# Optimization experiments

Measured on AMD Instinct MI355X. Metric: run time of the kernel, lower is better.

## Reference

```python
import jax, jax.numpy as jnp
import numpy as np

NEG_SLOPE = 0.2   # PyG GATConv leaky_relu slope
BN_EPS = 1e-5
N_NODES, N_EDGES = 50000, 800000
HEADS, CH, EDGE_DIM, K = 4, 64, 3, 4


def _bn(x):
    # BatchNorm1d in training mode, gamma=1, beta=0 (init defaults)
    mu = x.mean(axis=0)
    var = x.var(axis=0)
    return (x - mu) / jnp.sqrt(var + BN_EPS)


def _gat(x, src, dst, ea, W, a_src, a_dst, We, a_edge, bias, heads, out_ch):
    """PyG-style GATConv with edge features, add_self_loops=True (fill_value='mean')."""
    N = x.shape[0]
    E = src.shape[0]
    # self-loop edge_attr = scatter-mean of edge_attr by dst
    deg = jax.ops.segment_sum(jnp.ones((E,), x.dtype), dst, num_segments=N)
    ea_loop = jax.ops.segment_sum(ea, dst, num_segments=N) / jnp.maximum(deg, 1.0)[:, None]
    loop = jnp.arange(N)
    src2 = jnp.concatenate([src, loop])
    dst2 = jnp.concatenate([dst, loop])
    ea2 = jnp.concatenate([ea, ea_loop], axis=0)          # (E+N, edge_dim)
    h = (x @ W).reshape(N, heads, out_ch)                  # (N,H,C)
    a_s = (h * a_src).sum(-1)                              # (N,H)
    a_d = (h * a_dst).sum(-1)                              # (N,H)
    eh = (ea2 @ We).reshape(-1, heads, out_ch)             # (E+N,H,C)
    a_e = (eh * a_edge).sum(-1)                            # (E+N,H)
    logit = jax.nn.leaky_relu(a_s[src2] + a_d[dst2] + a_e, NEG_SLOPE)
    m = jax.lax.stop_gradient(jax.ops.segment_max(logit, dst2, num_segments=N))
    ex = jnp.exp(logit - m[dst2])
    den = jax.ops.segment_sum(ex, dst2, num_segments=N)
    alpha = ex / (den[dst2] + 1e-16)                       # segment softmax over dst
    out = jax.ops.segment_sum(alpha[:, :, None] * h[src2], dst2, num_segments=N)
    return out.reshape(N, heads * out_ch) + bias


def setup_inputs() -> dict:
    key = jax.random.key(0)
    ks = jax.random.split(key, 24)
    N, E, H, C, ED = N_NODES, N_EDGES, HEADS, CH, EDGE_DIM

    def g(k, shape, s=0.05):
        return jax.random.normal(k, shape, jnp.float32) * s

    return {
        "x": jax.random.normal(ks[0], (N, 2), jnp.float32),
        "edge_index": jax.random.randint(ks[1], (2, E), 0, N),
        "edge_attr": jax.random.normal(ks[2], (E, ED), jnp.float32),
        "Wp": g(ks[3], (2, C)), "bp": jnp.zeros((C,), jnp.float32),
        "W1": g(ks[4], (C, H * C)), "as1": g(ks[5], (H, C)), "ad1": g(ks[6], (H, C)),
        "We1": g(ks[7], (ED, H * C)), "ae1": g(ks[8], (H, C)), "b1": jnp.zeros((H * C,), jnp.float32),
        "W2": g(ks[9], (H * C, H * C)), "as2": g(ks[10], (H, C)), "ad2": g(ks[11], (H, C)),
        "We2": g(ks[12], (ED, H * C)), "ae2": g(ks[13], (H, C)), "b2": jnp.zeros((H * C,), jnp.float32),
        "W3": g(ks[14], (H * C, C)), "as3": g(ks[15], (1, C)), "ad3": g(ks[16], (1, C)),
        "We3": g(ks[17], (ED, C)), "ae3": g(ks[18], (1, C)), "b3": jnp.zeros((C,), jnp.float32),
        "Wc": g(ks[19], (C, K)), "bc": jnp.zeros((K,), jnp.float32),
    }


def reference(x, edge_index, edge_attr, Wp, bp,
              W1, as1, ad1, We1, ae1, b1,
              W2, as2, ad2, We2, ae2, b2,
              W3, as3, ad3, We3, ae3, b3,
              Wc, bc):
    src, dst = edge_index[0], edge_index[1]
    h = jax.nn.elu(_bn(x @ Wp + bp))
    h = jax.nn.elu(_bn(_gat(h, src, dst, edge_attr, W1, as1, ad1, We1, ae1, b1, HEADS, CH)))
    h = jax.nn.elu(_bn(_gat(h, src, dst, edge_attr, W2, as2, ad2, We2, ae2, b2, HEADS, CH)))
    h = jax.nn.elu(_gat(h, src, dst, edge_attr, W3, as3, ad3, We3, ae3, b3, 1, CH))
    logits = h @ Wc + bc
    return jax.nn.softmax(logits / 1.0, axis=-1)  # temperature = 1.0
```

## Files before the change

kernel.cpp:

```cpp
#include <hip/hip_runtime.h>
#include <hip/hip_fp16.h>
#include <math.h>

#define NN 50000
#define NE 800000
#define NEG 0.2f
#define EPS_BN 1e-5f
#define NROW 8192
#define NB_SC ((NN + 255) / 256)

typedef _Float16 f16x8 __attribute__((ext_vector_type(8)));
typedef float f32x4 __attribute__((ext_vector_type(4)));

struct __align__(16) Edge { int s; float e0, e1, e2; };

__device__ __forceinline__ float lrelu(float x){ return x > 0.f ? x : NEG * x; }
__device__ __forceinline__ float elu(float x){ return x > 0.f ? x : expm1f(x); }

__global__ __launch_bounds__(256) void k_deg(const int* __restrict__ dst, int* __restrict__ deg){
  int e = blockIdx.x * 256 + threadIdx.x;
  if (e >= NE) return;
  atomicAdd(&deg[dst[e]], 1);
}

__global__ __launch_bounds__(256) void k_scan1(const int* __restrict__ deg, int* __restrict__ bsum){
  __shared__ int sd[4];
  int t = threadIdx.x;
  int i = blockIdx.x * 256 + t;
  int v = (i < NN) ? deg[i] : 0;
  int s = v;
#pragma unroll
  for (int off = 32; off; off >>= 1) s += __shfl_down(s, off, 64);
  if ((t & 63) == 0) sd[t >> 6] = s;
  __syncthreads();
  if (t == 0) bsum[blockIdx.x] = sd[0] + sd[1] + sd[2] + sd[3];
}

__global__ __launch_bounds__(256) void k_scan2(int* __restrict__ bsum, int* __restrict__ rowptr){
  __shared__ int sm[256];
  int t = threadIdx.x;
  int v = (t < NB_SC) ? bsum[t] : 0;
  sm[t] = v;
  __syncthreads();
  for (int off = 1; off < 256; off <<= 1){
    int p = (t >= off) ? sm[t - off] : 0;
    __syncthreads();
    sm[t] += p;
    __syncthreads();
  }
  if (t < NB_SC) bsum[t] = sm[t] - v;
  if (t == 0) rowptr[NN] = NE;
}

__global__ __launch_bounds__(256) void k_scan3(const int* __restrict__ deg, const int* __restrict__ bsum,
                                               int* __restrict__ rowptr){
  __shared__ int sm[256];
  int t = threadIdx.x;
  int i = blockIdx.x * 256 + t;
  int v = (i < NN) ? deg[i] : 0;
  sm[t] = v;
  __syncthreads();
  for (int off = 1; off < 256; off <<= 1){
    int p = (t >= off) ? sm[t - off] : 0;
    __syncthreads();
    sm[t] += p;
    __syncthreads();
  }
  if (i < NN) rowptr[i] = bsum[blockIdx.x] + sm[t] - v;
}

__global__ __launch_bounds__(256) void k_fill(const int* __restrict__ src, const int* __restrict__ dst,
                                              const float* __restrict__ ea, const int* __restrict__ rowptr,
                                              int* __restrict__ cnt, Edge* __restrict__ edges){
  int e = blockIdx.x * 256 + threadIdx.x;
  if (e >= NE) return;
  int d = dst[e];
  int pos = rowptr[d] + atomicAdd(&cnt[d], 1);
  Edge ed;
  ed.s = src[e];
  ed.e0 = ea[e*3+0]; ed.e1 = ea[e*3+1]; ed.e2 = ea[e*3+2];
  edges[pos] = ed;
}

__global__ __launch_bounds__(256) void k_easum(const int* __restrict__ rowptr, const Edge* __restrict__ edges,
                                               float* __restrict__ easum){
  int n = blockIdx.x * 4 + (threadIdx.x >> 6);
  int c = threadIdx.x & 63;
  if (n >= NN) return;
  int start = rowptr[n], end = rowptr[n + 1];
  float s0 = 0.f, s1 = 0.f, s2 = 0.f;
  for (int p = start + c; p < end; p += 64){
    Edge e = edges[p];
    s0 += e.e0; s1 += e.e1; s2 += e.e2;
  }
#pragma unroll
  for (int off = 32; off; off >>= 1){
    s0 += __shfl_down(s0, off, 64);
    s1 += __shfl_down(s1, off, 64);
    s2 += __shfl_down(s2, off, 64);
  }
  if (c == 0){ easum[n*3+0] = s0; easum[n*3+1] = s1; easum[n*3+2] = s2; }
}

__global__ __launch_bounds__(256) void k_proj(const float* __restrict__ x, const float* __restrict__ Wp,
                                              const float* __restrict__ bp, float* __restrict__ h0){
  int i = blockIdx.x * 256 + threadIdx.x;
  if (i >= NN * 64) return;
  int n = i >> 6, c = i & 63;
  h0[i] = fmaf(x[n*2+0], Wp[c], fmaf(x[n*2+1], Wp[64+c], bp[c]));
}

template<int F>
__global__ void k_bn_stats(const float* __restrict__ x, float* __restrict__ ps, float* __restrict__ pq){
  int t = threadIdx.x;
  float s = 0.f, s2 = 0.f;
  for (int n = blockIdx.x; n < NN; n += 512){
    float v = x[(long)n * F + t];
    s += v; s2 += v * v;
  }
  ps[blockIdx.x * F + t] = s;
  pq[blockIdx.x * F + t] = s2;
}

template<int F>
__global__ void k_bn_fin(const float* __restrict__ ps, const float* __restrict__ pq,
                         float* __restrict__ mu, float* __restrict__ rs){
  int t = threadIdx.x;
  float s = 0.f, s2 = 0.f;
  for (int b = 0; b < 512; b++){ s += ps[b * F + t]; s2 += pq[b * F + t]; }
  float m = s * (1.f / NN);
  float var = s2 * (1.f / NN) - m * m;
  mu[t] = m;
  rs[t] = rsqrtf(var + EPS_BN);
}

__global__ __launch_bounds__(256) void k_wt(const float* __restrict__ W, __half* __restrict__ Wt,
                                            int K, int J){
  int t = blockIdx.x * 256 + threadIdx.x;
  if (t >= K * J) return;
  int k = t / J, j = t % J;
  Wt[(long)j * K + k] = __float2half(W[t]);
}

template<int H>
__global__ void k_edge_g(const float* __restrict__ We, const float* __restrict__ ae, float* __restrict__ g){
  int t = threadIdx.x;
  int h = t >> 6, c = t & 63;
  float a = ae[t];
  for (int d = 0; d < 3; d++){
    float p = We[d * (H*64) + t] * a;
    for (int off = 32; off; off >>= 1) p += __shfl_down(p, off, 64);
    if (c == 0) g[d * H + h] = p;
  }
  (void)h;
}

template<int K, int J>
__global__ __launch_bounds__(256) void k_gemm_mfma(const float* __restrict__ A, const __half* __restrict__ Wt,
                                                   const float* __restrict__ mu, const float* __restrict__ rs,
                                                   const float* __restrict__ asrc, const float* __restrict__ adst,
                                                   __half* __restrict__ C, float* __restrict__ aS,
                                                   float* __restrict__ aD){
  constexpr int NS = J / 16;
  constexpr int KT = K / 32;
  constexpr int HH = J / 64;
  __shared__ __half Bs[J][40];
  int t = threadIdx.x;
  int w = t >> 6;
  int l = t & 63;
  int row0 = blockIdx.x * 64;
  int lr = l & 15;
  int lg = l >> 4;

  f32x4 acc[NS];
#pragma unroll
  for (int s = 0; s < NS; s++) acc[s] = (f32x4){0.f, 0.f, 0.f, 0.f};

  int arow = row0 + w * 16 + lr;
  bool aval = arow < NN;
  const float* Arow = A + (long)arow * K;

  auto loadA = [&](int kt) -> f16x8 {
    f16x8 r;
#pragma unroll
    for (int k = 0; k < 8; k++) r[k] = (_Float16)0.f;
    if (aval){
      int k0 = kt * 32 + lg * 8;
      float4 q0 = *(const float4*)&Arow[k0];
      float4 q1 = *(const float4*)&Arow[k0 + 4];
      float4 m0 = *(const float4*)&mu[k0];
      float4 m1 = *(const float4*)&mu[k0 + 4];
      float4 r0 = *(const float4*)&rs[k0];
      float4 r1 = *(const float4*)&rs[k0 + 4];
      r[0] = (_Float16)elu((q0.x - m0.x) * r0.x);
      r[1] = (_Float16)elu((q0.y - m0.y) * r0.y);
      r[2] = (_Float16)elu((q0.z - m0.z) * r0.z);
      r[3] = (_Float16)elu((q0.w - m0.w) * r0.w);
      r[4] = (_Float16)elu((q1.x - m1.x) * r1.x);
      r[5] = (_Float16)elu((q1.y - m1.y) * r1.y);
      r[6] = (_Float16)elu((q1.z - m1.z) * r1.z);
      r[7] = (_Float16)elu((q1.w - m1.w) * r1.w);
    }
    return r;
  };

  f16x8 af_cur = loadA(0);

  for (int kt = 0; kt < KT; kt++){
    int kk = kt * 32;
#pragma unroll
    for (int i = 0; i < J / 64; i++){
      int ch = t + 256 * i;
      int c = ch >> 2, q = ch & 3;
      *(uint4*)&Bs[c][q * 8] = *(const uint4*)(Wt + (long)c * K + kk + q * 8);
    }
    __syncthreads();
    f16x8 af_nxt;
#pragma unroll
    for (int k = 0; k < 8; k++) af_nxt[k] = (_Float16)0.f;
    if (kt + 1 < KT) af_nxt = loadA(kt + 1);
#pragma unroll
    for (int s = 0; s < NS; s++){
      f16x8 bf = *(const f16x8*)&Bs[s * 16 + lr][lg * 8];
      acc[s] = __builtin_amdgcn_mfma_f32_16x16x32_f16(af_cur, bf, acc[s], 0, 0, 0);
    }
    __syncthreads();
    af_cur = af_nxt;
  }

  int orow = row0 + w * 16 + lg * 4;
  float sA[HH][4], dA[HH][4];
#pragma unroll
  for (int hd = 0; hd < HH; hd++)
#pragma unroll
    for (int i = 0; i < 4; i++){ sA[hd][i] = 0.f; dA[hd][i] = 0.f; }

#pragma unroll
  for (int s = 0; s < NS; s++){
    int cidx = s * 16 + lr;
    int hd = s >> 2;
    float a1 = asrc[cidx], a2 = adst[cidx];
#pragma unroll
    for (int i = 0; i < 4; i++){
      float v = acc[s][i];
      sA[hd][i] = fmaf(v, a1, sA[hd][i]);
      dA[hd][i] = fmaf(v, a2, dA[hd][i]);
      int r = orow + i;
      if (r < NN) C[(long)r * J + cidx] = __float2half(v);
    }
  }
#pragma unroll
  for (int off = 1; off <= 8; off <<= 1){
#pragma unroll
    for (int hd = 0; hd < HH; hd++)
#pragma unroll
      for (int i = 0; i < 4; i++){
        sA[hd][i] += __shfl_xor(sA[hd][i], off, 64);
        dA[hd][i] += __shfl_xor(dA[hd][i], off, 64);
      }
  }
  if (lr == 0){
#pragma unroll
    for (int i = 0; i < 4; i++){
      int r = orow + i;
      if (r < NN){
#pragma unroll
        for (int hd = 0; hd < HH; hd++){
          aS[r * HH + hd] = sA[hd][i];
          aD[r * HH + hd] = dA[hd][i];
        }
      }
    }
  }
}

__global__ __launch_bounds__(256) void k_gatn(const int* __restrict__ rowptr, const Edge* __restrict__ edges,
                                              const int* __restrict__ deg, const float* __restrict__ easum,
                                              const float* __restrict__ aS, const float* __restrict__ aD,
                                              const float* __restrict__ g4, const __half* __restrict__ hh,
                                              const float* __restrict__ bias, float* __restrict__ out){
  const int W = 256;
  int wid = threadIdx.x >> 6;
  int lane = threadIdx.x & 63;
  int row = blockIdx.x * 4 + wid;
  int e4 = lane >> 2, hl = lane & 3;
  int es = lane >> 5, ch8 = lane & 31;
  int c = ch8 * 8;
  int h2 = ch8 >> 3;
  float g0 = g4[0*4+hl], g1 = g4[1*4+hl], g2 = g4[2*4+hl];
  float4 bb0 = *(const float4*)&bias[c];
  float4 bb1 = *(const float4*)&bias[c+4];

  for (int n = row; n < NN; n += NROW){
    int start = rowptr[n], end = rowptr[n+1];
    float adn = aD[n*4+hl];
    float dg = (float)deg[n];
    float inv = 1.f / fmaxf(dg, 1.f);
    float ll = aS[n*4+hl] + adn + g0*(easum[n*3+0]*inv) + g1*(easum[n*3+1]*inv) + g2*(easum[n*3+2]*inv);
    ll = lrelu(ll);
    float evl = __expf(ll);
    float evl2 = __shfl(evl, h2, 64);
    f16x8 sv = *(const f16x8*)(hh + (long)n * W + c);
    float acc[8];
#pragma unroll
    for (int k = 0; k < 8; k++) acc[k] = (es == 0) ? evl2 * (float)sv[k] : 0.f;
    float denp = (lane < 4) ? evl : 0.f;

    for (int b0 = start; b0 < end; b0 += 16){
      int len = end - b0; if (len > 16) len = 16;
      float ev = 0.f; unsigned pk = 0;
      if (e4 < len){
        Edge e = edges[b0 + e4];
        float l = lrelu(aS[e.s*4+hl] + adn + g0*e.e0 + g1*e.e1 + g2*e.e2);
        ev = __expf(l);
        pk = ((unsigned)e.s << 16) | (unsigned)__half_as_ushort(__float2half(ev));
      }
      denp += ev;
      int iters = (len + 1) >> 1;
      for (int i = 0; i < iters; i++){
        int j = i * 2 + es;
        bool valid = j < len;
        int jj = valid ? j : 0;
        unsigned pj = __shfl((int)pk, jj * 4 + h2, 64);
        float aj = valid ? __half2float(__ushort_as_half((unsigned short)(pj & 0xffffu))) : 0.f;
        int sj = (int)(pj >> 16);
        f16x8 v = *(const f16x8*)(hh + (long)sj * W + c);
#pragma unroll
        for (int k = 0; k < 8; k++) acc[k] = fmaf(aj, (float)v[k], acc[k]);
      }
    }
#pragma unroll
    for (int off = 4; off <= 32; off <<= 1) denp += __shfl_xor(denp, off, 64);
    float den2 = __shfl(denp, h2, 64);
#pragma unroll
    for (int k = 0; k < 8; k++) acc[k] += __shfl_xor(acc[k], 32, 64);
    if (es == 0){
      float invd = 1.f / (den2 + 1e-16f);
      float o[8];
      o[0] = fmaf(acc[0], invd, bb0.x); o[1] = fmaf(acc[1], invd, bb0.y);
      o[2] = fmaf(acc[2], invd, bb0.z); o[3] = fmaf(acc[3], invd, bb0.w);
      o[4] = fmaf(acc[4], invd, bb1.x); o[5] = fmaf(acc[5], invd, bb1.y);
      o[6] = fmaf(acc[6], invd, bb1.z); o[7] = fmaf(acc[7], invd, bb1.w);
      *(float4*)&out[(long)n * W + c]     = make_float4(o[0], o[1], o[2], o[3]);
      *(float4*)&out[(long)n * W + c + 4] = make_float4(o[4], o[5], o[6], o[7]);
    }
  }
}

template<int H, bool ELU>
__global__ __launch_bounds__(256) void k_gatw(const int* __restrict__ rowptr, const Edge* __restrict__ edges,
                                              const int* __restrict__ deg, const float* __restrict__ easum,
                                              const float* __restrict__ aS, const float* __restrict__ aD,
                                              const float* __restrict__ g, const __half* __restrict__ hh,
                                              const float* __restrict__ bias, float* __restrict__ out){
  constexpr int W = H * 64;
  int wid = threadIdx.x >> 6;
  int lane = threadIdx.x & 63;
  int n = blockIdx.x * 4 + wid;
  int h = 0;
  if (n >= NN) return;
  int start = rowptr[n], end = rowptr[n + 1];
  float g0 = g[0*H+h], g1 = g[1*H+h], g2 = g[2*H+h];
  float adn = aD[n*H+h];
  int ch8 = lane >> 3;
  int es = lane & 7;

  float dg = (float)deg[n];
  float inv = 1.f / fmaxf(dg, 1.f);
  float ll = aS[n*H+h] + adn + g0*(easum[n*3+0]*inv) + g1*(easum[n*3+1]*inv) + g2*(easum[n*3+2]*inv);
  ll = lrelu(ll);
  float evl = __expf(ll);
  f16x8 sv = *(const f16x8*)(hh + (long)n * W + h * 64 + ch8 * 8);
  float acc[8];
#pragma unroll
  for (int k = 0; k < 8; k++) acc[k] = (es == 0) ? evl * (float)sv[k] : 0.f;
  float denp = (lane == 0) ? evl : 0.f;

  for (int base0 = start; base0 < end; base0 += 64){
    int len = end - base0; if (len > 64) len = 64;
    float ev = 0.f;
    unsigned pk = 0;
    if (lane < len){
      Edge e = edges[base0 + lane];
      float l = lrelu(aS[e.s*H+h] + adn + g0*e.e0 + g1*e.e1 + g2*e.e2);
      ev = __expf(l);
      pk = ((unsigned)e.s << 16) | (unsigned)__half_as_ushort(__float2half(ev));
    }
    denp += ev;
    for (int j = es; j < len; j += 8){
      unsigned pj = __shfl((int)pk, j, 64);
      float aj = __half2float(__ushort_as_half((unsigned short)(pj & 0xffffu)));
      int sj = (int)(pj >> 16);
      f16x8 v = *(const f16x8*)(hh + (long)sj * W + h * 64 + ch8 * 8);
#pragma unroll
      for (int k = 0; k < 8; k++) acc[k] = fmaf(aj, (float)v[k], acc[k]);
    }
  }

#pragma unroll
  for (int off = 32; off; off >>= 1) denp += __shfl_xor(denp, off, 64);
#pragma unroll
  for (int k = 0; k < 8; k++){
    acc[k] += __shfl_xor(acc[k], 1, 64);
    acc[k] += __shfl_xor(acc[k], 2, 64);
    acc[k] += __shfl_xor(acc[k], 4, 64);
  }
  if (es == 0){
    float invden = 1.f / (denp + 1e-16f);
    int cb = h * 64 + ch8 * 8;
    float4 b0 = *(const float4*)&bias[cb];
    float4 b1 = *(const float4*)&bias[cb + 4];
    float bb[8] = {b0.x, b0.y, b0.z, b0.w, b1.x, b1.y, b1.z, b1.w};
#pragma unroll
    for (int k = 0; k < 8; k++){
      acc[k] = acc[k] * invden + bb[k];
      if (ELU) acc[k] = acc[k] > 0.f ? acc[k] : expm1f(acc[k]);
    }
    float4 o0 = make_float4(acc[0], acc[1], acc[2], acc[3]);
    float4 o1 = make_float4(acc[4], acc[5], acc[6], acc[7]);
    *(float4*)&out[(long)n * W + cb] = o0;
    *(float4*)&out[(long)n * W + cb + 4] = o1;
  }
}

__global__ __launch_bounds__(64) void k_final(const float* __restrict__ h3, const float* __restrict__ Wc,
                                              const float* __restrict__ bc, float* __restrict__ out){
  int n = blockIdx.x;
  int c = threadIdx.x;
  float v = h3[(long)n * 64 + c];
  float r0 = v * Wc[c*4+0], r1 = v * Wc[c*4+1], r2 = v * Wc[c*4+2], r3 = v * Wc[c*4+3];
  for (int off = 32; off; off >>= 1){
    r0 += __shfl_down(r0, off, 64);
    r1 += __shfl_down(r1, off, 64);
    r2 += __shfl_down(r2, off, 64);
    r3 += __shfl_down(r3, off, 64);
  }
  if (c == 0){
    r0 += bc[0]; r1 += bc[1]; r2 += bc[2]; r3 += bc[3];
    float mm = fmaxf(fmaxf(r0, r1), fmaxf(r2, r3));
    float e0 = __expf(r0 - mm), e1 = __expf(r1 - mm), e2 = __expf(r2 - mm), e3 = __expf(r3 - mm);
    float is = 1.f / (e0 + e1 + e2 + e3);
    out[n*4+0] = e0 * is; out[n*4+1] = e1 * is; out[n*4+2] = e2 * is; out[n*4+3] = e3 * is;
  }
}

extern "C" void kernel_launch(void* const* d_in, const int* in_sizes, int n_in,
                              void* d_out, int out_size, void* d_ws, size_t ws_size,
                              hipStream_t stream){
  const float* x   = (const float*)d_in[0];
  const int*   ei  = (const int*)d_in[1];
  const float* ea  = (const float*)d_in[2];
  const float* Wp  = (const float*)d_in[3];
  const float* bp  = (const float*)d_in[4];
  const float* W1  = (const float*)d_in[5];
  const float* as1 = (const float*)d_in[6];
  const float* ad1 = (const float*)d_in[7];
  const float* We1 = (const float*)d_in[8];
  const float* ae1 = (const float*)d_in[9];
  const float* b1  = (const float*)d_in[10];
  const float* W2  = (const float*)d_in[11];
  const float* as2 = (const float*)d_in[12];
  const float* ad2 = (const float*)d_in[13];
  const float* We2 = (const float*)d_in[14];
  const float* ae2 = (const float*)d_in[15];
  const float* b2  = (const float*)d_in[16];
  const float* W3  = (const float*)d_in[17];
  const float* as3 = (const float*)d_in[18];
  const float* ad3 = (const float*)d_in[19];
  const float* We3 = (const float*)d_in[20];
  const float* ae3 = (const float*)d_in[21];
  const float* b3  = (const float*)d_in[22];
  const float* Wc  = (const float*)d_in[23];
  const float* bc  = (const float*)d_in[24];
  const int* srcI = ei;
  const int* dstI = ei + NE;

  char* base = (char*)d_ws;
  size_t off = 0;
  auto alloc = [&](size_t bytes) -> void* {
    void* p = base + off;
    off += (bytes + 255) & ~(size_t)255;
    return p;
  };
  float*  bufA  = (float*)alloc((size_t)NN * 256 * 4);
  __half* hB    = (__half*)alloc((size_t)NN * 256 * 2);
  __half* Wt1   = (__half*)alloc((size_t)64 * 256 * 2);
  __half* Wt2   = (__half*)alloc((size_t)256 * 256 * 2);
  __half* Wt3   = (__half*)alloc((size_t)256 * 64 * 2);
  int*   deg   = (int*)  alloc((size_t)NN * 4);
  int*   cnt   = (int*)  alloc((size_t)NN * 4);
  int*   rowptr= (int*)  alloc((size_t)(NN + 1) * 4);
  int*   bsum  = (int*)  alloc((size_t)NB_SC * 4);
  Edge*  edges = (Edge*) alloc((size_t)NE * sizeof(Edge));
  float* easum = (float*)alloc((size_t)NN * 3 * 4);
  float* aS    = (float*)alloc((size_t)NN * 4 * 4);
  float* aD    = (float*)alloc((size_t)NN * 4 * 4);
  float* g     = (float*)alloc(256);
  float* pbs   = (float*)alloc((size_t)512 * 256 * 4);
  float* pbq   = (float*)alloc((size_t)512 * 256 * 4);
  float* bmu   = (float*)alloc(256 * 4);
  float* brs   = (float*)alloc(256 * 4);
  (void)ws_size; (void)in_sizes; (void)n_in; (void)out_size;

  hipMemsetAsync(deg, 0, (size_t)NN * 4, stream);
  hipMemsetAsync(cnt, 0, (size_t)NN * 4, stream);
  k_deg<<<(NE + 255) / 256, 256, 0, stream>>>(dstI, deg);
  k_scan1<<<NB_SC, 256, 0, stream>>>(deg, bsum);
  k_scan2<<<1, 256, 0, stream>>>(bsum, rowptr);
  k_scan3<<<NB_SC, 256, 0, stream>>>(deg, bsum, rowptr);
  k_fill<<<(NE + 255) / 256, 256, 0, stream>>>(srcI, dstI, ea, rowptr, cnt, edges);
  k_easum<<<(NN + 3) / 4, 256, 0, stream>>>(rowptr, edges, easum);
  k_wt<<<(64 * 256 + 255) / 256, 256, 0, stream>>>(W1, Wt1, 64, 256);
  k_wt<<<(256 * 256 + 255) / 256, 256, 0, stream>>>(W2, Wt2, 256, 256);
  k_wt<<<(256 * 64 + 255) / 256, 256, 0, stream>>>(W3, Wt3, 256, 64);

  k_proj<<<(NN * 64 + 255) / 256, 256, 0, stream>>>(x, Wp, bp, bufA);
  k_bn_stats<64><<<512, 64, 0, stream>>>(bufA, pbs, pbq);
  k_bn_fin<64><<<1, 64, 0, stream>>>(pbs, pbq, bmu, brs);

  k_edge_g<4><<<1, 256, 0, stream>>>(We1, ae1, g);
  k_gemm_mfma<64, 256><<<(NN + 63) / 64, 256, 0, stream>>>(bufA, Wt1, bmu, brs, as1, ad1, hB, aS, aD);
  k_gatn<<<NROW / 4, 256, 0, stream>>>(rowptr, edges, deg, easum, aS, aD, g, hB, b1, bufA);
  k_bn_stats<256><<<512, 256, 0, stream>>>(bufA, pbs, pbq);
  k_bn_fin<256><<<1, 256, 0, stream>>>(pbs, pbq, bmu, brs);

  k_edge_g<4><<<1, 256, 0, stream>>>(We2, ae2, g);
  k_gemm_mfma<256, 256><<<(NN + 63) / 64, 256, 0, stream>>>(bufA, Wt2, bmu, brs, as2, ad2, hB, aS, aD);
  k_gatn<<<NROW / 4, 256, 0, stream>>>(rowptr, edges, deg, easum, aS, aD, g, hB, b2, bufA);
  k_bn_stats<256><<<512, 256, 0, stream>>>(bufA, pbs, pbq);
  k_bn_fin<256><<<1, 256, 0, stream>>>(pbs, pbq, bmu, brs);

  k_edge_g<1><<<1, 64, 0, stream>>>(We3, ae3, g);
  k_gemm_mfma<256, 64><<<(NN + 63) / 64, 256, 0, stream>>>(bufA, Wt3, bmu, brs, as3, ad3, hB, aS, aD);
  k_gatw<1, true><<<(NN + 3) / 4, 256, 0, stream>>>(rowptr, edges, deg, easum, aS, aD, g, hB, b3, bufA);

  k_final<<<NN, 64, 0, stream>>>(bufA, Wc, bc, (float*)d_out);
}
```

Baseline: 550.3 us.

## Fuse BatchNorm statistics into GAT aggregation kernel and merge weight transposes

Each GAT aggregation kernel now accumulates per-channel sum and sum-of-squares of its outputs, reduces them across the block's waves in shared memory, and writes per-block partials. A new parallel finalize kernel (one block per channel) reduces those partials into mean and rsqrt variance. This removes the separate BN-stats pass that re-read the 50000x256 fp32 output after each of the first two GAT layers. The three weight-transpose launches are also merged into one. The cost is extra registers in the GAT kernel and a larger partial buffer to reduce.

After: 500.3 us. -9.1%, faster.

```diff
diff --git a/kernel.cpp b/kernel.cpp
--- a/kernel.cpp
+++ b/kernel.cpp
@@ -7,6 +7,7 @@
 #define NEG 0.2f
 #define EPS_BN 1e-5f
 #define NROW 8192
+#define NGB  (NROW / 4)
 #define NB_SC ((NN + 255) / 256)
 
 typedef _Float16 f16x8 __attribute__((ext_vector_type(8)));
@@ -134,12 +135,43 @@
   rs[t] = rsqrtf(var + EPS_BN);
 }
 
-__global__ __launch_bounds__(256) void k_wt(const float* __restrict__ W, __half* __restrict__ Wt,
-                                            int K, int J){
+__global__ __launch_bounds__(256) void k_bn_fin2048(const float* __restrict__ pbs, const float* __restrict__ pbq,
+                                                    float* __restrict__ mu, float* __restrict__ rs){
+  __shared__ float sd[2][4];
+  int c = blockIdx.x;
+  int t = threadIdx.x;
+  float s = 0.f, q = 0.f;
+  for (int i = t; i < NGB; i += 256){ s += pbs[c * NGB + i]; q += pbq[c * NGB + i]; }
+#pragma unroll
+  for (int off = 32; off; off >>= 1){ s += __shfl_down(s, off, 64); q += __shfl_down(q, off, 64); }
+  if ((t & 63) == 0){ sd[0][t >> 6] = s; sd[1][t >> 6] = q; }
+  __syncthreads();
+  if (t == 0){
+    s = sd[0][0] + sd[0][1] + sd[0][2] + sd[0][3];
+    q = sd[1][0] + sd[1][1] + sd[1][2] + sd[1][3];
+    float m = s * (1.f / NN);
+    float var = q * (1.f / NN) - m * m;
+    mu[c] = m;
+    rs[c] = rsqrtf(var + EPS_BN);
+  }
+}
+
+__global__ __launch_bounds__(256) void k_wt3(const float* __restrict__ W1, const float* __restrict__ W2,
+                                             const float* __restrict__ W3, __half* __restrict__ Wt1,
+                                             __half* __restrict__ Wt2, __half* __restrict__ Wt3){
   int t = blockIdx.x * 256 + threadIdx.x;
-  if (t >= K * J) return;
-  int k = t / J, j = t % J;
-  Wt[(long)j * K + k] = __float2half(W[t]);
+  if (t < 64 * 256){
+    int k = t / 256, j = t % 256;
+    Wt1[(long)j * 64 + k] = __float2half(W1[t]);
+  }
+  if (t < 256 * 256){
+    int k = t / 256, j = t % 256;
+    Wt2[(long)j * 256 + k] = __float2half(W2[t]);
+  }
+  if (t < 256 * 64){
+    int k = t / 64, j = t % 64;
+    Wt3[(long)j * 256 + k] = __float2half(W3[t]);
+  }
 }
 
 template<int H>
@@ -274,11 +306,13 @@
   }
 }
 
+template<bool STATS>
 __global__ __launch_bounds__(256) void k_gatn(const int* __restrict__ rowptr, const Edge* __restrict__ edges,
                                               const int* __restrict__ deg, const float* __restrict__ easum,
                                               const float* __restrict__ aS, const float* __restrict__ aD,
                                               const float* __restrict__ g4, const __half* __restrict__ hh,
-                                              const float* __restrict__ bias, float* __restrict__ out){
+                                              const float* __restrict__ bias, float* __restrict__ out,
+                                              float* __restrict__ pbs, float* __restrict__ pbq){
   const int W = 256;
   int wid = threadIdx.x >> 6;
   int lane = threadIdx.x & 63;
@@ -290,6 +324,11 @@
   float g0 = g4[0*4+hl], g1 = g4[1*4+hl], g2 = g4[2*4+hl];
   float4 bb0 = *(const float4*)&bias[c];
   float4 bb1 = *(const float4*)&bias[c+4];
+  float sum8[8], sq8[8];
+  if (STATS){
+#pragma unroll
+    for (int k = 0; k < 8; k++){ sum8[k] = 0.f; sq8[k] = 0.f; }
+  }
 
   for (int n = row; n < NN; n += NROW){
     int start = rowptr[n], end = rowptr[n+1];
@@ -341,9 +380,28 @@
       o[2] = fmaf(acc[2], invd, bb0.z); o[3] = fmaf(acc[3], invd, bb0.w);
       o[4] = fmaf(acc[4], invd, bb1.x); o[5] = fmaf(acc[5], invd, bb1.y);
       o[6] = fmaf(acc[6], invd, bb1.z); o[7] = fmaf(acc[7], invd, bb1.w);
+      if (STATS){
+#pragma unroll
+        for (int k = 0; k < 8; k++){ sum8[k] += o[k]; sq8[k] += o[k]*o[k]; }
+      }
       *(float4*)&out[(long)n * W + c]     = make_float4(o[0], o[1], o[2], o[3]);
       *(float4*)&out[(long)n * W + c + 4] = make_float4(o[4], o[5], o[6], o[7]);
     }
+  }
+
+  if (STATS){
+    __shared__ float ls[4][256];
+    __shared__ float lq[4][256];
+    if (es == 0){
+#pragma unroll
+      for (int k = 0; k < 8; k++){ ls[wid][c + k] = sum8[k]; lq[wid][c + k] = sq8[k]; }
+    }
+    __syncthreads();
+    int ch = threadIdx.x;
+    float s = ls[0][ch] + ls[1][ch] + ls[2][ch] + ls[3][ch];
+    float q = lq[0][ch] + lq[1][ch] + lq[2][ch] + lq[3][ch];
+    pbs[ch * NGB + blockIdx.x] = s;
+    pbq[ch * NGB + blockIdx.x] = q;
   }
 }
 
@@ -496,8 +554,8 @@
   float* aS    = (float*)alloc((size_t)NN * 4 * 4);
   float* aD    = (float*)alloc((size_t)NN * 4 * 4);
   float* g     = (float*)alloc(256);
-  float* pbs   = (float*)alloc((size_t)512 * 256 * 4);
-  float* pbq   = (float*)alloc((size_t)512 * 256 * 4);
+  float* pbs   = (float*)alloc((size_t)256 * NGB * 4);
+  float* pbq   = (float*)alloc((size_t)256 * NGB * 4);
   float* bmu   = (float*)alloc(256 * 4);
   float* brs   = (float*)alloc(256 * 4);
   (void)ws_size; (void)in_sizes; (void)n_in; (void)out_size;
@@ -510,9 +568,7 @@
   k_scan3<<<NB_SC, 256, 0, stream>>>(deg, bsum, rowptr);
   k_fill<<<(NE + 255) / 256, 256, 0, stream>>>(srcI, dstI, ea, rowptr, cnt, edges);
   k_easum<<<(NN + 3) / 4, 256, 0, stream>>>(rowptr, edges, easum);
-  k_wt<<<(64 * 256 + 255) / 256, 256, 0, stream>>>(W1, Wt1, 64, 256);
-  k_wt<<<(256 * 256 + 255) / 256, 256, 0, stream>>>(W2, Wt2, 256, 256);
-  k_wt<<<(256 * 64 + 255) / 256, 256, 0, stream>>>(W3, Wt3, 256, 64);
+  k_wt3<<<(256 * 256 + 255) / 256, 256, 0, stream>>>(W1, W2, W3, Wt1, Wt2, Wt3);
 
   k_proj<<<(NN * 64 + 255) / 256, 256, 0, stream>>>(x, Wp, bp, bufA);
   k_bn_stats<64><<<512, 64, 0, stream>>>(bufA, pbs, pbq);
@@ -520,15 +576,13 @@
 
   k_edge_g<4><<<1, 256, 0, stream>>>(We1, ae1, g);
   k_gemm_mfma<64, 256><<<(NN + 63) / 64, 256, 0, stream>>>(bufA, Wt1, bmu, brs, as1, ad1, hB, aS, aD);
-  k_gatn<<<NROW / 4, 256, 0, stream>>>(rowptr, edges, deg, easum, aS, aD, g, hB, b1, bufA);
-  k_bn_stats<256><<<512, 256, 0, stream>>>(bufA, pbs, pbq);
-  k_bn_fin<256><<<1, 256, 0, stream>>>(pbs, pbq, bmu, brs);
+  k_gatn<true><<<NGB, 256, 0, stream>>>(rowptr, edges, deg, easum, aS, aD, g, hB, b1, bufA, pbs, pbq);
+  k_bn_fin2048<<<256, 256, 0, stream>>>(pbs, pbq, bmu, brs);
 
   k_edge_g<4><<<1, 256, 0, stream>>>(We2, ae2, g);
   k_gemm_mfma<256, 256><<<(NN + 63) / 64, 256, 0, stream>>>(bufA, Wt2, bmu, brs, as2, ad2, hB, aS, aD);
-  k_gatn<<<NROW / 4, 256, 0, stream>>>(rowptr, edges, deg, easum, aS, aD, g, hB, b2, bufA);
-  k_bn_stats<256><<<512, 256, 0, stream>>>(bufA, pbs, pbq);
-  k_bn_fin<256><<<1, 256, 0, stream>>>(pbs, pbq, bmu, brs);
+  k_gatn<true><<<NGB, 256, 0, stream>>>(rowptr, edges, deg, easum, aS, aD, g, hB, b2, bufA, pbs, pbq);
+  k_bn_fin2048<<<256, 256, 0, stream>>>(pbs, pbq, bmu, brs);
 
   k_edge_g<1><<<1, 64, 0, stream>>>(We3, ae3, g);
   k_gemm_mfma<256, 64><<<(NN + 63) / 64, 256, 0, stream>>>(bufA, Wt3, bmu, brs, as3, ad3, hB, aS, aD);
```
